# Performance work log

Hardware: AMD Instinct MI355X
Metric: run time of the kernel (lower is better)

## Reference

```python
import jax, jax.numpy as jnp
import numpy as np

# init constants: mul_vals=[1565,1342], shift_vals=[8,8]; module adds +7 to shifts
M0 = 1565
M1 = 1342
S0 = 8 + 7  # 15
S1 = 8 + 7  # 15


def _requant(x, m, s):
    # x * m, add rounding offset 1<<(s-1), truncate-to-int (torch LongTensor cast
    # truncates toward zero, matching astype on these positive-rounded values),
    # arithmetic right shift by s, clamp to [0, 255], back to float32.
    y = x * jnp.float32(m)
    y = (y + jnp.float32(1 << (s - 1))).astype(jnp.int64)
    y = jnp.right_shift(y, s).astype(jnp.float32)
    return jnp.clip(y, 0.0, 255.0)


def setup_inputs() -> dict:
    key = jax.random.key(0)
    k1, k2, k3, k4, k5 = jax.random.split(key, 5)
    B = 1048576
    X = jax.random.normal(k1, (B, 117), dtype=jnp.float32)
    W1 = jax.random.normal(k2, (20, 117), dtype=jnp.float32) * 0.1
    b1 = jax.random.normal(k3, (20,), dtype=jnp.float32) * 0.1
    W2 = jax.random.normal(k4, (2, 20), dtype=jnp.float32) * 0.1
    b2 = jax.random.normal(k5, (2,), dtype=jnp.float32) * 0.1
    return {"X": X, "W1": W1, "b1": b1, "W2": W2, "b2": b2}


def reference(X, W1, b1, W2, b2):
    # linear1: [B,117] @ [117,20] + b1
    h = jnp.einsum("bi,oi->bo", X, W1) + b1
    h = _requant(h, M0, S0)  # quantized ReLU-like clamp to [0,255]
    # linear2: [B,20] @ [20,2] + b2
    o = jnp.einsum("bi,oi->bo", h, W2) + b2
    o = _requant(o, M1, S1)
    return o
```

## Files before the change

kernel.cpp:

```cpp
#include <hip/hip_runtime.h>

#define COLS 117
#define NOUT1 20
#define ROWS 64
#define NV (ROWS * COLS / 4)
#define REM (NV - 7 * 256)
#define PSTR 21
#define PFROW (ROWS * PSTR)

__device__ __forceinline__ float requant(float x, float m, float off, int s) {
  float y = __fmul_rn(x, m);
  y = __fadd_rn(y, off);
  long long yi = (long long)y;
  yi >>= s;
  float r = (float)yi;
  return fminf(fmaxf(r, 0.0f), 255.0f);
}

__global__ void transpose_w1(const float* __restrict__ W1, float* __restrict__ w1t) {
  for (int idx = threadIdx.x; idx < NOUT1 * COLS; idx += blockDim.x) {
    int o = idx / COLS, k = idx % COLS;
    w1t[k * NOUT1 + o] = W1[idx];
  }
}

template <bool TW>
__global__ __launch_bounds__(256, 5) void fann_kernel(
    const float* __restrict__ X, const float* __restrict__ W1,
    const float* __restrict__ b1, const float* __restrict__ W2,
    const float* __restrict__ b2, float* __restrict__ out) {
  __shared__ __align__(16) float xs[ROWS * COLS];
  float4* xs4 = (float4*)xs;
  const int t = threadIdx.x;
  {
    const float4* __restrict__ src =
        reinterpret_cast<const float4*>(X) + (size_t)blockIdx.x * NV;
    #pragma unroll
    for (int i = 0; i < 7; ++i)
      __builtin_amdgcn_global_load_lds(
          (const __attribute__((address_space(1))) void*)&src[t + i * 256],
          (__attribute__((address_space(3))) void*)&xs4[t + i * 256], 16, 0, 0);
    if (t < REM)
      __builtin_amdgcn_global_load_lds(
          (const __attribute__((address_space(1))) void*)&src[t + 7 * 256],
          (__attribute__((address_space(3))) void*)&xs4[t + 7 * 256], 16, 0, 0);
  }
  __syncthreads();

  const int w = __builtin_amdgcn_readfirstlane(t >> 6);
  const int l = t & 63;
  const int k0 = w * 29;
  const int kn = (w == 3) ? 30 : 29;

  float acc[NOUT1];
  #pragma unroll
  for (int o = 0; o < NOUT1; ++o) acc[o] = 0.0f;
  const float* xr = xs + l * COLS + k0;

  if (TW) {
    const float4* __restrict__ w4 =
        reinterpret_cast<const float4*>(W1) + (size_t)k0 * (NOUT1 / 4);
    for (int kk = 0; kk < kn; ++kk) {
      float x = xr[kk];
      #pragma unroll
      for (int j = 0; j < 5; ++j) {
        float4 wv = w4[kk * 5 + j];
        acc[4 * j + 0] = fmaf(x, wv.x, acc[4 * j + 0]);
        acc[4 * j + 1] = fmaf(x, wv.y, acc[4 * j + 1]);
        acc[4 * j + 2] = fmaf(x, wv.z, acc[4 * j + 2]);
        acc[4 * j + 3] = fmaf(x, wv.w, acc[4 * j + 3]);
      }
    }
  } else {
    for (int kk = 0; kk < kn; ++kk) {
      float x = xr[kk];
      #pragma unroll
      for (int o = 0; o < NOUT1; ++o)
        acc[o] = fmaf(x, W1[o * COLS + k0 + kk], acc[o]);
    }
  }
  __syncthreads();

  {
    float* pw = xs + w * PFROW + l * PSTR;
    #pragma unroll
    for (int o = 0; o < NOUT1; ++o) pw[o] = acc[o];
  }
  __syncthreads();

  {
    const int r  = (w << 4) + (l & 15);
    const int og = l >> 4;
    float g0 = 0.0f, g1 = 0.0f;
    #pragma unroll
    for (int j = 0; j < 5; ++j) {
      const int o = og * 5 + j;
      const float* pa = xs + r * PSTR + o;
      float h = pa[0 * PFROW] + pa[1 * PFROW] + pa[2 * PFROW] + pa[3 * PFROW];
      h += b1[o];
      float hq = requant(h, 1565.0f, 16384.0f, 15);
      g0 = fmaf(hq, W2[o], g0);
      g1 = fmaf(hq, W2[NOUT1 + o], g1);
    }
    const int lb = l & 15;
    float a01 = __shfl(g0, lb + 16);
    float a02 = __shfl(g0, lb + 32);
    float a03 = __shfl(g0, lb + 48);
    float a11 = __shfl(g1, lb + 16);
    float a12 = __shfl(g1, lb + 32);
    float a13 = __shfl(g1, lb + 48);
    if (og == 0) {
      float s0 = ((g0 + a01) + a02) + a03 + b2[0];
      float s1 = ((g1 + a11) + a12) + a13 + b2[1];
      float2 res;
      res.x = requant(s0, 1342.0f, 16384.0f, 15);
      res.y = requant(s1, 1342.0f, 16384.0f, 15);
      reinterpret_cast<float2*>(out)[(size_t)blockIdx.x * ROWS + r] = res;
    }
  }
}

__global__ void fann_tail(const float* __restrict__ X, const float* __restrict__ W1,
                          const float* __restrict__ b1, const float* __restrict__ W2,
                          const float* __restrict__ b2, float* __restrict__ out,
                          int start, int B) {
  int row = start + blockIdx.x * blockDim.x + threadIdx.x;
  if (row >= B) return;
  float acc[NOUT1];
  #pragma unroll
  for (int o = 0; o < NOUT1; ++o) acc[o] = b1[o];
  const float* xr = X + (size_t)row * COLS;
  for (int k = 0; k < COLS; ++k) {
    float x = xr[k];
    #pragma unroll
    for (int o = 0; o < NOUT1; ++o) acc[o] = fmaf(x, W1[o * COLS + k], acc[o]);
  }
  float s0 = b2[0], s1 = b2[1];
  #pragma unroll
  for (int o = 0; o < NOUT1; ++o) {
    float hq = requant(acc[o], 1565.0f, 16384.0f, 15);
    s0 = fmaf(hq, W2[o], s0);
    s1 = fmaf(hq, W2[NOUT1 + o], s1);
  }
  out[(size_t)row * 2 + 0] = requant(s0, 1342.0f, 16384.0f, 15);
  out[(size_t)row * 2 + 1] = requant(s1, 1342.0f, 16384.0f, 15);
}

extern "C" void kernel_launch(void* const* d_in, const int* in_sizes, int n_in,
                              void* d_out, int out_size, void* d_ws, size_t ws_size,
                              hipStream_t stream) {
  const float* X  = (const float*)d_in[0];
  const float* W1 = (const float*)d_in[1];
  const float* b1 = (const float*)d_in[2];
  const float* W2 = (const float*)d_in[3];
  const float* b2 = (const float*)d_in[4];
  float* out = (float*)d_out;
  const int B = in_sizes[0] / COLS;
  const int nblk = B / ROWS;
  const int tail = B - nblk * ROWS;

  const bool useT = ws_size >= (size_t)(COLS * NOUT1 * sizeof(float));
  if (useT) {
    float* w1t = (float*)d_ws;
    transpose_w1<<<1, 256, 0, stream>>>(W1, w1t);
    if (nblk > 0)
      fann_kernel<true><<<nblk, 256, 0, stream>>>(X, w1t, b1, W2, b2, out);
  } else {
    if (nblk > 0)
      fann_kernel<false><<<nblk, 256, 0, stream>>>(X, W1, b1, W2, b2, out);
  }
  if (tail > 0)
    fann_tail<<<(tail + 63) / 64, 64, 0, stream>>>(X, W1, b1, W2, b2, out,
                                                   nblk * ROWS, B);
}
```

Measured before the change: 110.7 us.

## Convert to persistent grid with double-buffered LDS prefetch of X tiles

Launches a fixed grid of 512 persistent blocks that loop over row tiles, issuing async global-to-LDS loads for the next tile before computing the current one. Explicit vmcnt waits and raw barriers replace __syncthreads. The partial-sum reduction now uses a separate two-slot buffer with an accumulate step. This aims to hide load latency and cut block launch overhead, at the cost of lower occupancy (launch bounds 2) and fewer outstanding memory requests per CU.

```diff
diff --git a/kernel.cpp b/kernel.cpp
--- a/kernel.cpp
+++ b/kernel.cpp
@@ -4,9 +4,19 @@
 #define NOUT1 20
 #define ROWS 64
 #define NV (ROWS * COLS / 4)
-#define REM (NV - 7 * 256)
+#define NVPAD 2048
 #define PSTR 21
-#define PFROW (ROWS * PSTR)
+#define GRID 512
+
+#define VM_WAIT8() asm volatile("s_waitcnt vmcnt(8)" ::: "memory")
+#define VM_WAIT0() asm volatile("s_waitcnt vmcnt(0)" ::: "memory")
+#define LGKM0()    asm volatile("s_waitcnt lgkmcnt(0)" ::: "memory")
+#define RAW_BAR()                          \
+  do {                                     \
+    __builtin_amdgcn_sched_barrier(0);     \
+    __builtin_amdgcn_s_barrier();          \
+    __builtin_amdgcn_sched_barrier(0);     \
+  } while (0)
 
 __device__ __forceinline__ float requant(float x, float m, float off, int s) {
   float y = __fmul_rn(x, m);
@@ -24,98 +34,115 @@
   }
 }
 
+__device__ __forceinline__ void stage_tile(float4* dst, const float4* src, int t) {
+#pragma unroll
+  for (int i = 0; i < 7; ++i)
+    __builtin_amdgcn_global_load_lds(
+        (const __attribute__((address_space(1))) void*)(src + t + i * 256),
+        (__attribute__((address_space(3))) void*)(dst + t + i * 256), 16, 0, 0);
+  const int i8 = t + 7 * 256;
+  const float4* s8 = src + (i8 < NV ? i8 : 0);
+  __builtin_amdgcn_global_load_lds(
+      (const __attribute__((address_space(1))) void*)s8,
+      (__attribute__((address_space(3))) void*)(dst + i8), 16, 0, 0);
+}
+
 template <bool TW>
-__global__ __launch_bounds__(256, 5) void fann_kernel(
+__global__ __launch_bounds__(256, 2) void fann_pipe(
     const float* __restrict__ X, const float* __restrict__ W1,
     const float* __restrict__ b1, const float* __restrict__ W2,
-    const float* __restrict__ b2, float* __restrict__ out) {
-  __shared__ __align__(16) float xs[ROWS * COLS];
-  float4* xs4 = (float4*)xs;
+    const float* __restrict__ b2, float* __restrict__ out, int ntiles) {
+  __shared__ __align__(16) float4 buf[2][NVPAD];
+  __shared__ float P[2][ROWS * PSTR];
   const int t = threadIdx.x;
-  {
-    const float4* __restrict__ src =
-        reinterpret_cast<const float4*>(X) + (size_t)blockIdx.x * NV;
-    #pragma unroll
-    for (int i = 0; i < 7; ++i)
-      __builtin_amdgcn_global_load_lds(
-          (const __attribute__((address_space(1))) void*)&src[t + i * 256],
-          (__attribute__((address_space(3))) void*)&xs4[t + i * 256], 16, 0, 0);
-    if (t < REM)
-      __builtin_amdgcn_global_load_lds(
-          (const __attribute__((address_space(1))) void*)&src[t + 7 * 256],
-          (__attribute__((address_space(3))) void*)&xs4[t + 7 * 256], 16, 0, 0);
-  }
-  __syncthreads();
-
   const int w = __builtin_amdgcn_readfirstlane(t >> 6);
   const int l = t & 63;
   const int k0 = w * 29;
   const int kn = (w == 3) ? 30 : 29;
-
-  float acc[NOUT1];
-  #pragma unroll
-  for (int o = 0; o < NOUT1; ++o) acc[o] = 0.0f;
-  const float* xr = xs + l * COLS + k0;
-
-  if (TW) {
-    const float4* __restrict__ w4 =
-        reinterpret_cast<const float4*>(W1) + (size_t)k0 * (NOUT1 / 4);
-    for (int kk = 0; kk < kn; ++kk) {
-      float x = xr[kk];
-      #pragma unroll
+  const int G = gridDim.x;
+  const float4* __restrict__ Xv = reinterpret_cast<const float4*>(X);
+
+  int tile = blockIdx.x;
+  int cur = 0;
+  if (tile < ntiles) stage_tile(buf[0], Xv + (size_t)tile * NV, t);
+
+  for (; tile < ntiles; tile += G, cur ^= 1) {
+    const int nt = tile + G;
+    const bool pf = (nt < ntiles);
+    if (pf) stage_tile(buf[cur ^ 1], Xv + (size_t)nt * NV, t);
+    if (pf) VM_WAIT8(); else VM_WAIT0();
+    RAW_BAR();
+
+    float acc[NOUT1];
+#pragma unroll
+    for (int o = 0; o < NOUT1; ++o) acc[o] = 0.0f;
+    const float* xr = (const float*)buf[cur] + l * COLS + k0;
+    if (TW) {
+      const float4* __restrict__ w4 =
+          reinterpret_cast<const float4*>(W1) + (size_t)k0 * (NOUT1 / 4);
+      for (int kk = 0; kk < kn; ++kk) {
+        float x = xr[kk];
+#pragma unroll
+        for (int j = 0; j < 5; ++j) {
+          float4 wv = w4[kk * 5 + j];
+          acc[4 * j + 0] = fmaf(x, wv.x, acc[4 * j + 0]);
+          acc[4 * j + 1] = fmaf(x, wv.y, acc[4 * j + 1]);
+          acc[4 * j + 2] = fmaf(x, wv.z, acc[4 * j + 2]);
+          acc[4 * j + 3] = fmaf(x, wv.w, acc[4 * j + 3]);
+        }
+      }
+    } else {
+      for (int kk = 0; kk < kn; ++kk) {
+        float x = xr[kk];
+#pragma unroll
+        for (int o = 0; o < NOUT1; ++o)
+          acc[o] = fmaf(x, W1[o * COLS + k0 + kk], acc[o]);
+      }
+    }
+
+    if (w < 2) {
+      float* pw = P[w] + l * PSTR;
+#pragma unroll
+      for (int o = 0; o < NOUT1; ++o) pw[o] = acc[o];
+    }
+    LGKM0();
+    RAW_BAR();
+    if (w >= 2) {
+      float* pw = P[w - 2] + l * PSTR;
+#pragma unroll
+      for (int o = 0; o < NOUT1; ++o) pw[o] += acc[o];
+    }
+    LGKM0();
+    RAW_BAR();
+
+    {
+      const int r = (w << 4) + (l & 15);
+      const int og = l >> 4;
+      float g0 = 0.0f, g1 = 0.0f;
+#pragma unroll
       for (int j = 0; j < 5; ++j) {
-        float4 wv = w4[kk * 5 + j];
-        acc[4 * j + 0] = fmaf(x, wv.x, acc[4 * j + 0]);
-        acc[4 * j + 1] = fmaf(x, wv.y, acc[4 * j + 1]);
-        acc[4 * j + 2] = fmaf(x, wv.z, acc[4 * j + 2]);
-        acc[4 * j + 3] = fmaf(x, wv.w, acc[4 * j + 3]);
-      }
-    }
-  } else {
-    for (int kk = 0; kk < kn; ++kk) {
-      float x = xr[kk];
-      #pragma unroll
-      for (int o = 0; o < NOUT1; ++o)
-        acc[o] = fmaf(x, W1[o * COLS + k0 + kk], acc[o]);
-    }
-  }
-  __syncthreads();
-
-  {
-    float* pw = xs + w * PFROW + l * PSTR;
-    #pragma unroll
-    for (int o = 0; o < NOUT1; ++o) pw[o] = acc[o];
-  }
-  __syncthreads();
-
-  {
-    const int r  = (w << 4) + (l & 15);
-    const int og = l >> 4;
-    float g0 = 0.0f, g1 = 0.0f;
-    #pragma unroll
-    for (int j = 0; j < 5; ++j) {
-      const int o = og * 5 + j;
-      const float* pa = xs + r * PSTR + o;
-      float h = pa[0 * PFROW] + pa[1 * PFROW] + pa[2 * PFROW] + pa[3 * PFROW];
-      h += b1[o];
-      float hq = requant(h, 1565.0f, 16384.0f, 15);
-      g0 = fmaf(hq, W2[o], g0);
-      g1 = fmaf(hq, W2[NOUT1 + o], g1);
-    }
-    const int lb = l & 15;
-    float a01 = __shfl(g0, lb + 16);
-    float a02 = __shfl(g0, lb + 32);
-    float a03 = __shfl(g0, lb + 48);
-    float a11 = __shfl(g1, lb + 16);
-    float a12 = __shfl(g1, lb + 32);
-    float a13 = __shfl(g1, lb + 48);
-    if (og == 0) {
-      float s0 = ((g0 + a01) + a02) + a03 + b2[0];
-      float s1 = ((g1 + a11) + a12) + a13 + b2[1];
-      float2 res;
-      res.x = requant(s0, 1342.0f, 16384.0f, 15);
-      res.y = requant(s1, 1342.0f, 16384.0f, 15);
-      reinterpret_cast<float2*>(out)[(size_t)blockIdx.x * ROWS + r] = res;
+        const int o = og * 5 + j;
+        float h = P[0][r * PSTR + o] + P[1][r * PSTR + o];
+        h += b1[o];
+        float hq = requant(h, 1565.0f, 16384.0f, 15);
+        g0 = fmaf(hq, W2[o], g0);
+        g1 = fmaf(hq, W2[NOUT1 + o], g1);
+      }
+      const int lb = l & 15;
+      float a01 = __shfl(g0, lb + 16);
+      float a02 = __shfl(g0, lb + 32);
+      float a03 = __shfl(g0, lb + 48);
+      float a11 = __shfl(g1, lb + 16);
+      float a12 = __shfl(g1, lb + 32);
+      float a13 = __shfl(g1, lb + 48);
+      if (og == 0) {
+        float s0 = ((g0 + a01) + a02) + a03 + b2[0];
+        float s1 = ((g1 + a11) + a12) + a13 + b2[1];
+        float2 res;
+        res.x = requant(s0, 1342.0f, 16384.0f, 15);
+        res.y = requant(s1, 1342.0f, 16384.0f, 15);
+        reinterpret_cast<float2*>(out)[(size_t)tile * ROWS + r] = res;
+      }
     }
   }
 }
@@ -127,16 +154,16 @@
   int row = start + blockIdx.x * blockDim.x + threadIdx.x;
   if (row >= B) return;
   float acc[NOUT1];
-  #pragma unroll
+#pragma unroll
   for (int o = 0; o < NOUT1; ++o) acc[o] = b1[o];
   const float* xr = X + (size_t)row * COLS;
   for (int k = 0; k < COLS; ++k) {
     float x = xr[k];
-    #pragma unroll
+#pragma unroll
     for (int o = 0; o < NOUT1; ++o) acc[o] = fmaf(x, W1[o * COLS + k], acc[o]);
   }
   float s0 = b2[0], s1 = b2[1];
-  #pragma unroll
+#pragma unroll
   for (int o = 0; o < NOUT1; ++o) {
     float hq = requant(acc[o], 1565.0f, 16384.0f, 15);
     s0 = fmaf(hq, W2[o], s0);
@@ -156,20 +183,21 @@
   const float* b2 = (const float*)d_in[4];
   float* out = (float*)d_out;
   const int B = in_sizes[0] / COLS;
-  const int nblk = B / ROWS;
-  const int tail = B - nblk * ROWS;
+  const int ntiles = B / ROWS;
+  const int tail = B - ntiles * ROWS;
+  const int grid = (ntiles < GRID) ? (ntiles > 0 ? ntiles : 1) : GRID;
 
   const bool useT = ws_size >= (size_t)(COLS * NOUT1 * sizeof(float));
   if (useT) {
     float* w1t = (float*)d_ws;
     transpose_w1<<<1, 256, 0, stream>>>(W1, w1t);
-    if (nblk > 0)
-      fann_kernel<true><<<nblk, 256, 0, stream>>>(X, w1t, b1, W2, b2, out);
+    if (ntiles > 0)
+      fann_pipe<true><<<grid, 256, 0, stream>>>(X, w1t, b1, W2, b2, out, ntiles);
   } else {
-    if (nblk > 0)
-      fann_kernel<false><<<nblk, 256, 0, stream>>>(X, W1, b1, W2, b2, out);
+    if (ntiles > 0)
+      fann_pipe<false><<<grid, 256, 0, stream>>>(X, W1, b1, W2, b2, out, ntiles);
   }
   if (tail > 0)
     fann_tail<<<(tail + 63) / 64, 64, 0, stream>>>(X, W1, b1, W2, b2, out,
-                                                   nblk * ROWS, B);
-}
+                                                   ntiles * ROWS, B);
+}
```

New measurement: 163.2 us. 47.4% more time.
